# Kernel tuning notes

Measured on AMD Instinct MI355X. Metric: run time of the kernel, lower is better.

The kernel has to match this reference:

```python
import jax, jax.numpy as jnp
import numpy as np

B, T, H = 2, 2048, 1024
DFF = 4 * H        # dense_mlp hidden width
E = 8              # num_experts_temp
TOP_K = 2


def setup_inputs() -> dict:
    key = jax.random.key(0)
    ks = jax.random.split(key, 6)
    s_h = 1.0 / np.sqrt(H)
    s_f = 1.0 / np.sqrt(DFF)
    return {
        "hidden_states": jax.random.normal(ks[0], (B, T, H), dtype=jnp.float32),
        "router_w": jax.random.normal(ks[1], (E, H), dtype=jnp.float32) * s_h,
        "w1": jax.random.normal(ks[2], (E, H, DFF), dtype=jnp.float32) * s_h,
        "b1": jnp.zeros((E, DFF), dtype=jnp.float32),
        "w2": jax.random.normal(ks[3], (E, DFF, H), dtype=jnp.float32) * s_f,
        "b2": jnp.zeros((E, H), dtype=jnp.float32),
    }


def reference(hidden_states, router_w, w1, b1, w2, b2):
    # Router: [B,T,E]
    router_logits = jnp.einsum("bth,eh->bte", hidden_states, router_w)
    topk_vals, topk_idx = jax.lax.top_k(router_logits, TOP_K)        # [B,T,K]
    topk_w = jax.nn.softmax(topk_vals.astype(jnp.float32), axis=-1)
    topk_w = topk_w.astype(hidden_states.dtype)

    # Dense compute of ALL experts (faithful to the original module).
    h = jnp.einsum("bth,ehf->btef", hidden_states, w1) + b1          # [B,T,E,DFF]
    h = jax.nn.gelu(h)
    expert_out = jnp.einsum("btef,efh->bteh", h, w2) + b2            # [B,T,E,H]

    # Gather top-k experts per token and mix.
    topk_out = jnp.take_along_axis(expert_out, topk_idx[..., None], axis=2)  # [B,T,K,H]
    mixed = jnp.sum(topk_out * topk_w[..., None], axis=2)            # [B,T,H]
    return mixed
```

## Files before the change

kernel.cpp:

```cpp
#include <hip/hip_runtime.h>
#include <hip/hip_bf16.h>
#include <stdint.h>

#define AS1 __attribute__((address_space(1)))
#define AS3 __attribute__((address_space(3)))

typedef __bf16 bf16x8 __attribute__((ext_vector_type(8)));
typedef float floatx4 __attribute__((ext_vector_type(4)));

static constexpr int NTOK = 4096;
static constexpr int H    = 1024;
static constexpr int DFF  = 4096;
static constexpr int E    = 8;
static constexpr int BN   = 128;
static constexpr int RB   = 71;

static constexpr size_t OFF_XCS    = 0;
static constexpr size_t OFF_HS     = 18874368;
static constexpr size_t OFF_P      = 94371840;
static constexpr size_t PSZ        = 18874368;
static constexpr size_t OFF_RTIDX  = 169869312;
static constexpr size_t OFF_RTW    = 169902080;
static constexpr size_t OFF_PTOK   = 169934848;
static constexpr size_t OFF_TOKPOS = 169971712;
static constexpr size_t OFF_CNT    = 170004480;
static constexpr size_t WS_NEED    = 170004608;

__device__ __forceinline__ unsigned short f2bf(float f) {
    __bf16 b = (__bf16)f;
    return __builtin_bit_cast(unsigned short, b);
}
__device__ __forceinline__ float bf2f(unsigned short u) {
    unsigned int v = ((unsigned int)u) << 16;
    return __builtin_bit_cast(float, v);
}

__device__ __forceinline__ void gload16(const void* g, void* l) {
    __builtin_amdgcn_global_load_lds((AS1 void*)g, (AS3 void*)l, 16, 0, 0);
}

__device__ __forceinline__ int find_expert_tot(const int* __restrict__ counts, int row, int* tot_out) {
    int e = 0, tot = 0;
#pragma unroll
    for (int i = 0; i < E; ++i) {
        int c = (counts[i] + 127) & ~127;
        if (row >= tot + c) e = i + 1;
        tot += c;
    }
    *tot_out = tot;
    return e;
}
__device__ __forceinline__ int padded_prefix(const int* __restrict__ counts, int e) {
    int o = 0;
#pragma unroll
    for (int i = 0; i < E; ++i) {
        int c = (counts[i] + 127) & ~127;
        o += (i < e) ? c : 0;
    }
    return o;
}

__global__ __launch_bounds__(256) void k_router(const float* __restrict__ x,
                                                const float* __restrict__ rw,
                                                int* __restrict__ rt_idx,
                                                float* __restrict__ rt_w,
                                                int* __restrict__ counts) {
    const int wv = threadIdx.x >> 6, ln = threadIdx.x & 63;
    const int t = blockIdx.x * 4 + wv;
    const float* xr = x + (size_t)t * H + ln * 4;
    float4 xv[4];
#pragma unroll
    for (int c = 0; c < 4; ++c) xv[c] = *(const float4*)(xr + c * 256);
    float lg[E];
#pragma unroll
    for (int e = 0; e < E; ++e) {
        const float* rr = rw + (size_t)e * H + ln * 4;
        float acc = 0.f;
#pragma unroll
        for (int c = 0; c < 4; ++c) {
            float4 rv = *(const float4*)(rr + c * 256);
            acc += xv[c].x * rv.x + xv[c].y * rv.y + xv[c].z * rv.z + xv[c].w * rv.w;
        }
#pragma unroll
        for (int s = 32; s > 0; s >>= 1) acc += __shfl_xor(acc, s, 64);
        lg[e] = acc;
    }
    if (ln == 0) {
        int i0 = 0; float v0 = lg[0];
#pragma unroll
        for (int e = 1; e < E; ++e) if (lg[e] > v0) { v0 = lg[e]; i0 = e; }
        int i1 = -1; float v1 = -INFINITY;
#pragma unroll
        for (int e = 0; e < E; ++e) if (e != i0 && lg[e] > v1) { v1 = lg[e]; i1 = e; }
        float e1 = expf(v1 - v0);
        float inv = 1.f / (1.f + e1);
        rt_idx[2 * t] = i0; rt_idx[2 * t + 1] = i1;
        rt_w[2 * t] = inv;  rt_w[2 * t + 1] = e1 * inv;
        atomicAdd(&counts[i0], 1);
        atomicAdd(&counts[i1], 1);
    }
}

__global__ __launch_bounds__(256) void k_scatter(const int* __restrict__ rt_idx,
                                                 const int* __restrict__ counts,
                                                 int* __restrict__ cursors,
                                                 int* __restrict__ pair_tok,
                                                 int* __restrict__ tok_pos) {
    int t = blockIdx.x * 256 + threadIdx.x;
    if (t >= NTOK) return;
    for (int k = 0; k < 2; ++k) {
        int e = rt_idx[2 * t + k];
        int p = atomicAdd(&cursors[e], 1);
        int pos = padded_prefix(counts, e) + p;
        pair_tok[pos] = t;
        tok_pos[2 * t + k] = pos;
    }
}

__global__ __launch_bounds__(256) void k_gather(const float* __restrict__ x,
                                                const int* __restrict__ counts,
                                                const int* __restrict__ pair_tok,
                                                unsigned short* __restrict__ xcs) {
    int pos = blockIdx.x;
    int tot;
    int e = find_expert_tot(counts, pos, &tot);
    if (pos >= tot) return;
    int off_e = padded_prefix(counts, e);
    bool valid = (pos - off_e) < counts[e];
    int tok = valid ? pair_tok[pos] : 0;
    int k0 = threadIdx.x * 4;
    float4 xv = valid ? *(const float4*)(x + (size_t)tok * H + k0)
                      : make_float4(0.f, 0.f, 0.f, 0.f);
    ushort4 o;
    o.x = f2bf(xv.x); o.y = f2bf(xv.y); o.z = f2bf(xv.z); o.w = f2bf(xv.w);
    int rb = pos >> 7, m = pos & 127;
    size_t idx = (((size_t)(rb * 32 + (k0 >> 5)) * 128 + m) * 32) + (k0 & 31);
    *(ushort4*)(xcs + idx) = o;
}

__global__ __launch_bounds__(256) void k_gemm1(const unsigned short* __restrict__ Xc,
                                               const float* __restrict__ w1,
                                               const int* __restrict__ counts,
                                               const float* __restrict__ b1,
                                               unsigned short* __restrict__ Hs) {
    constexpr int KB = H / 32;
    constexpr int MP = 36;
    constexpr int NB = DFF / BN;
    constexpr int CPX = NB * RB / 8;
    const int bid = blockIdx.x;
    const int t = (bid & 7) * CPX + (bid >> 3);
    const int rb = t / NB;
    const int row = rb * 128;
    int tot;
    const int e = find_expert_tot(counts, row, &tot);
    if (row >= tot) return;
    const int n0 = (t % NB) * BN;

    __shared__ unsigned short smem[4 * 128 * MP];
    unsigned short* lds_a = smem;
    unsigned short* lds_b = smem + 4096;

    const int tid = threadIdx.x;
    const int wv = tid >> 6, ln = tid & 63;
    const int quad = ln >> 4, lr = ln & 15;
    const int wm = (wv & 1) * 64, wn = (wv >> 1) * 64;
    const int bswz = quad ^ ((lr >> 1) & 3);

    const int skq = wv, sn = ln;
    const int sswz = skq ^ ((sn >> 1) & 3);
    const int wb1 = sn * 32 + sswz * 8;
    const int wb2 = wb1 + 2048;

    floatx4 acc[4][4];
#pragma unroll
    for (int i = 0; i < 4; ++i)
#pragma unroll
        for (int j = 0; j < 4; ++j) acc[i][j] = (floatx4){0.f, 0.f, 0.f, 0.f};

    const unsigned short* Atile = Xc + (size_t)rb * KB * 4096;
    const float* Bsrc = w1 + ((size_t)e * H + skq * 8) * DFF + n0 + sn;

    float br[16];
#pragma unroll
    for (int j = 0; j < 8; ++j) {
        br[j]     = Bsrc[(size_t)j * DFF];
        br[8 + j] = Bsrc[(size_t)j * DFF + 64];
    }

    for (int kb = 0; kb < KB; ++kb) {
        __syncthreads();
        {
            union { unsigned short us[8]; uint4 v; } u1, u2;
#pragma unroll
            for (int j = 0; j < 8; ++j) { u1.us[j] = f2bf(br[j]); u2.us[j] = f2bf(br[8 + j]); }
            *(uint4*)(lds_b + wb1) = u1.v;
            *(uint4*)(lds_b + wb2) = u2.v;
        }
        const unsigned short* a_src = Atile + (size_t)kb * 4096 + (wv * 2) * 512 + ln * 8;
        gload16(a_src, &lds_a[(wv * 2) * 512]);
        gload16(a_src + 512, &lds_a[(wv * 2 + 1) * 512]);
        {
            const int kbn = (kb + 1 < KB) ? kb + 1 : kb;
            const float* bs = Bsrc + (size_t)kbn * 32 * DFF;
#pragma unroll
            for (int j = 0; j < 8; ++j) {
                br[j]     = bs[(size_t)j * DFF];
                br[8 + j] = bs[(size_t)j * DFF + 64];
            }
        }
        __syncthreads();
        bf16x8 af[4], bg[4];
#pragma unroll
        for (int i = 0; i < 4; ++i) {
            af[i] = *(const bf16x8*)(lds_a + (wm + i * 16 + lr) * 32 + quad * 8);
            bg[i] = *(const bf16x8*)(lds_b + (wn + i * 16 + lr) * 32 + bswz * 8);
        }
#pragma unroll
        for (int i = 0; i < 4; ++i)
#pragma unroll
            for (int j = 0; j < 4; ++j)
                acc[i][j] = __builtin_amdgcn_mfma_f32_16x16x32_bf16(af[i], bg[j], acc[i][j], 0, 0, 0);
    }

    float bj[4];
#pragma unroll
    for (int j = 0; j < 4; ++j) bj[j] = b1[(size_t)e * DFF + n0 + wn + j * 16 + lr];
    __syncthreads();
#pragma unroll
    for (int j = 0; j < 4; ++j) {
        const int fl = wn + j * 16 + lr;
        const int fb = fl >> 5, f5 = fl & 31;
        unsigned short* dst = smem + fb * (128 * MP) + f5;
#pragma unroll
        for (int i = 0; i < 4; ++i) {
#pragma unroll
            for (int r = 0; r < 4; ++r) {
                const int m = wm + i * 16 + quad * 4 + r;
                float v = acc[i][j][r] + bj[j];
                float u = 0.79788456080286535588f * (v + 0.044715f * v * v * v);
                float ez = __expf(2.f * u);
                float g = v * (1.f - 1.f / (ez + 1.f));
                dst[m * MP] = f2bf(g);
            }
        }
    }
    __syncthreads();
    const size_t hsbase = ((size_t)rb * 128 + (n0 >> 5)) * 4096;
#pragma unroll
    for (int it = 0; it < 8; ++it) {
        const int g = (it * 256 + tid) * 8;
        const int fb = g >> 12, rem = g & 4095, m = rem >> 5, f5 = rem & 31;
        const unsigned short* s = smem + fb * (128 * MP) + m * MP + f5;
        uint2 lo = *(const uint2*)s;
        uint2 hi = *(const uint2*)(s + 4);
        *(uint4*)(Hs + hsbase + (size_t)g) = make_uint4(lo.x, lo.y, hi.x, hi.y);
    }
}

__global__ __launch_bounds__(256) void k_gemm2(const unsigned short* __restrict__ Hs,
                                               const float* __restrict__ w2,
                                               const int* __restrict__ counts,
                                               const float* __restrict__ b2,
                                               unsigned short* __restrict__ Pb) {
    constexpr int KB = DFF / 32;
    constexpr int NSPLIT = 4;
    constexpr int KBS = KB / NSPLIT;
    constexpr int NB = H / BN;
    constexpr int CPX = NB * RB * NSPLIT / 8;
    const int bid = blockIdx.x;
    const int t = (bid & 7) * CPX + (bid >> 3);
    const int nb = t & 7;
    const int rest = t >> 3;
    const int rb = rest % RB;
    const int ks = rest / RB;
    const int row = rb * 128;
    int tot;
    const int e = find_expert_tot(counts, row, &tot);
    if (row >= tot) return;
    const int n0 = nb * BN;

    __shared__ unsigned short smem[8192];
    unsigned short* lds_a = smem;
    unsigned short* lds_b = smem + 4096;

    const int tid = threadIdx.x;
    const int wv = tid >> 6, ln = tid & 63;
    const int quad = ln >> 4, lr = ln & 15;
    const int wm = (wv & 1) * 64, wn = (wv >> 1) * 64;
    const int bswz = quad ^ ((lr >> 1) & 3);

    const int skq = wv, sn = ln;
    const int sswz = skq ^ ((sn >> 1) & 3);
    const int wb1 = sn * 32 + sswz * 8;
    const int wb2 = wb1 + 2048;

    floatx4 acc[4][4];
#pragma unroll
    for (int i = 0; i < 4; ++i)
#pragma unroll
        for (int j = 0; j < 4; ++j) acc[i][j] = (floatx4){0.f, 0.f, 0.f, 0.f};

    const unsigned short* Atile = Hs + ((size_t)rb * KB + ks * KBS) * 4096;
    const float* Bsrc = w2 + ((size_t)e * DFF + ks * KBS * 32 + skq * 8) * H + n0 + sn;

    float br[16];
#pragma unroll
    for (int j = 0; j < 8; ++j) {
        br[j]     = Bsrc[(size_t)j * H];
        br[8 + j] = Bsrc[(size_t)j * H + 64];
    }

    for (int kb = 0; kb < KBS; ++kb) {
        __syncthreads();
        {
            union { unsigned short us[8]; uint4 v; } u1, u2;
#pragma unroll
            for (int j = 0; j < 8; ++j) { u1.us[j] = f2bf(br[j]); u2.us[j] = f2bf(br[8 + j]); }
            *(uint4*)(lds_b + wb1) = u1.v;
            *(uint4*)(lds_b + wb2) = u2.v;
        }
        const unsigned short* a_src = Atile + (size_t)kb * 4096 + (wv * 2) * 512 + ln * 8;
        gload16(a_src, &lds_a[(wv * 2) * 512]);
        gload16(a_src + 512, &lds_a[(wv * 2 + 1) * 512]);
        {
            const int kbn = (kb + 1 < KBS) ? kb + 1 : kb;
            const float* bs = Bsrc + (size_t)kbn * 32 * H;
#pragma unroll
            for (int j = 0; j < 8; ++j) {
                br[j]     = bs[(size_t)j * H];
                br[8 + j] = bs[(size_t)j * H + 64];
            }
        }
        __syncthreads();
        bf16x8 af[4], bg[4];
#pragma unroll
        for (int i = 0; i < 4; ++i) {
            af[i] = *(const bf16x8*)(lds_a + (wm + i * 16 + lr) * 32 + quad * 8);
            bg[i] = *(const bf16x8*)(lds_b + (wn + i * 16 + lr) * 32 + bswz * 8);
        }
#pragma unroll
        for (int i = 0; i < 4; ++i)
#pragma unroll
            for (int j = 0; j < 4; ++j)
                acc[i][j] = __builtin_amdgcn_mfma_f32_16x16x32_bf16(af[i], bg[j], acc[i][j], 0, 0, 0);
    }

    float bj[4];
#pragma unroll
    for (int j = 0; j < 4; ++j)
        bj[j] = (ks == 0) ? b2[(size_t)e * H + n0 + wn + j * 16 + lr] : 0.f;
    unsigned short* P = Pb + (size_t)ks * (PSZ / 2);
#pragma unroll
    for (int i = 0; i < 4; ++i) {
#pragma unroll
        for (int r = 0; r < 4; ++r) {
            const int m = wm + i * 16 + quad * 4 + r;
            unsigned short* rowp = P + (size_t)(rb * 128 + m) * H + n0;
#pragma unroll
            for (int j = 0; j < 4; ++j)
                rowp[wn + j * 16 + lr] = f2bf(acc[i][j][r] + bj[j]);
        }
    }
}

__global__ __launch_bounds__(256) void k_mix(const unsigned short* __restrict__ Pb,
                                             const int* __restrict__ tok_pos,
                                             const float* __restrict__ rt_w,
                                             float* __restrict__ out) {
    const int t = blockIdx.x;
    const int c = threadIdx.x * 4;
    const int p0 = tok_pos[2 * t], p1 = tok_pos[2 * t + 1];
    const float w0 = rt_w[2 * t], w1 = rt_w[2 * t + 1];
    float4 s0 = make_float4(0.f, 0.f, 0.f, 0.f);
    float4 s1 = make_float4(0.f, 0.f, 0.f, 0.f);
#pragma unroll
    for (int q = 0; q < 4; ++q) {
        const unsigned short* P = Pb + (size_t)q * (PSZ / 2);
        ushort4 a = *(const ushort4*)(P + (size_t)p0 * H + c);
        ushort4 b = *(const ushort4*)(P + (size_t)p1 * H + c);
        s0.x += bf2f(a.x); s0.y += bf2f(a.y); s0.z += bf2f(a.z); s0.w += bf2f(a.w);
        s1.x += bf2f(b.x); s1.y += bf2f(b.y); s1.z += bf2f(b.z); s1.w += bf2f(b.w);
    }
    float4 o;
    o.x = w0 * s0.x + w1 * s1.x;
    o.y = w0 * s0.y + w1 * s1.y;
    o.z = w0 * s0.z + w1 * s1.z;
    o.w = w0 * s0.w + w1 * s1.w;
    *(float4*)(out + (size_t)t * H + c) = o;
}

extern "C" void kernel_launch(void* const* d_in, const int* in_sizes, int n_in,
                              void* d_out, int out_size, void* d_ws, size_t ws_size,
                              hipStream_t stream) {
    const float* x  = (const float*)d_in[0];
    const float* rw = (const float*)d_in[1];
    const float* w1 = (const float*)d_in[2];
    const float* b1 = (const float*)d_in[3];
    const float* w2 = (const float*)d_in[4];
    const float* b2 = (const float*)d_in[5];
    float* out = (float*)d_out;
    char* ws = (char*)d_ws;
    if (ws_size < WS_NEED) return;

    unsigned short* XcS = (unsigned short*)(ws + OFF_XCS);
    unsigned short* Hs  = (unsigned short*)(ws + OFF_HS);
    unsigned short* Pb  = (unsigned short*)(ws + OFF_P);
    int*   rt_idx   = (int*)(ws + OFF_RTIDX);
    float* rt_w     = (float*)(ws + OFF_RTW);
    int*   pair_tok = (int*)(ws + OFF_PTOK);
    int*   tok_pos  = (int*)(ws + OFF_TOKPOS);
    int*   cnt      = (int*)(ws + OFF_CNT);
    int*   cur      = cnt + 8;

    hipMemsetAsync(cnt, 0, 128, stream);

    k_router<<<NTOK / 4, 256, 0, stream>>>(x, rw, rt_idx, rt_w, cnt);
    k_scatter<<<NTOK / 256, 256, 0, stream>>>(rt_idx, cnt, cur, pair_tok, tok_pos);
    k_gather<<<RB * 128, 256, 0, stream>>>(x, cnt, pair_tok, XcS);

    k_gemm1<<<(DFF / BN) * RB, 256, 0, stream>>>(XcS, w1, cnt, b1, Hs);
    k_gemm2<<<(H / BN) * RB * 4, 256, 0, stream>>>(Hs, w2, cnt, b2, Pb);

    k_mix<<<NTOK, 256, 0, stream>>>(Pb, tok_pos, rt_w, out);
}
```

Baseline: 665.8 us.

## Double-buffer LDS tiles and register prefetch in both expert GEMM kernels

Replaces the single-buffered K-loop in both expert GEMMs with a ping-pong pipeline. Two LDS buffers hold A and B tiles, and two register sets hold prefetched fp32 weights. The next tile's A gload and B conversion/store overlap the MFMA compute on the current buffer, which halves the number of __syncthreads per K step. This doubles LDS use in gemm2 and raises register pressure, and both kernels now use a hardcoded trip count of 32 K-blocks.

```diff
diff --git a/kernel.cpp b/kernel.cpp
--- a/kernel.cpp
+++ b/kernel.cpp
@@ -138,6 +138,71 @@
     *(ushort4*)(xcs + idx) = o;
 }
 
+#define LOADB(SET, KBN) do {                                                   \
+    const float* bs_ = Bsrc + (size_t)(KBN) * 32 * LDB;                        \
+    _Pragma("unroll")                                                          \
+    for (int j_ = 0; j_ < 8; ++j_) {                                           \
+        brg[SET][j_]     = bs_[(size_t)j_ * LDB];                              \
+        brg[SET][8 + j_] = bs_[(size_t)j_ * LDB + 64];                         \
+    }                                                                          \
+} while (0)
+
+#define STOREB(SET, BUF) do {                                                  \
+    union { unsigned short us[8]; uint4 v; } u1_, u2_;                         \
+    _Pragma("unroll")                                                          \
+    for (int j_ = 0; j_ < 8; ++j_) {                                           \
+        u1_.us[j_] = f2bf(brg[SET][j_]);                                       \
+        u2_.us[j_] = f2bf(brg[SET][8 + j_]);                                   \
+    }                                                                          \
+    *(uint4*)(lds_b + (BUF) * 4096 + wb1) = u1_.v;                             \
+    *(uint4*)(lds_b + (BUF) * 4096 + wb2) = u2_.v;                             \
+} while (0)
+
+#define GLOADA(KB1, BUF) do {                                                  \
+    const unsigned short* a_ = Atile + (size_t)(KB1) * 4096 + (wv * 2) * 512 + ln * 8; \
+    gload16(a_, lds_a + (BUF) * 4096 + (wv * 2) * 512);                        \
+    gload16(a_ + 512, lds_a + (BUF) * 4096 + (wv * 2 + 1) * 512);              \
+} while (0)
+
+#define COMPUTE(BUF) do {                                                      \
+    bf16x8 af_[4], bg_[4];                                                     \
+    _Pragma("unroll")                                                          \
+    for (int i_ = 0; i_ < 4; ++i_) {                                           \
+        af_[i_] = *(const bf16x8*)(lds_a + (BUF) * 4096 + (wm + i_ * 16 + lr) * 32 + quad * 8); \
+        bg_[i_] = *(const bf16x8*)(lds_b + (BUF) * 4096 + (wn + i_ * 16 + lr) * 32 + bswz * 8); \
+    }                                                                          \
+    _Pragma("unroll")                                                          \
+    for (int i_ = 0; i_ < 4; ++i_)                                             \
+        _Pragma("unroll")                                                      \
+        for (int j_ = 0; j_ < 4; ++j_)                                         \
+            acc[i_][j_] = __builtin_amdgcn_mfma_f32_16x16x32_bf16(af_[i_], bg_[j_], acc[i_][j_], 0, 0, 0); \
+} while (0)
+
+#define GEMM_PIPELINE()                                                        \
+    LOADB(0, 0);                                                               \
+    STOREB(0, 0);                       \
+    GLOADA(0, 0);                                                              \
+    LOADB(1, 1);                                                               \
+    __syncthreads();                   \
+    for (int t2_ = 0; t2_ < 15; ++t2_) {                                       \
+        const int t_ = t2_ * 2;                                                \
+        GLOADA(t_ + 1, 1);            \
+        STOREB(1, 1);                            \
+        LOADB(0, t_ + 2);                               \
+        COMPUTE(0);                                               \
+        __syncthreads();                                                       \
+        GLOADA(t_ + 2, 0);                                                     \
+        STOREB(0, 0);                                                          \
+        LOADB(1, t_ + 3);                          \
+        COMPUTE(1);                                           \
+        __syncthreads();                                                       \
+    }                                                                          \
+    GLOADA(31, 1);                                                             \
+    STOREB(1, 1);                                          \
+    COMPUTE(0);                                                   \
+    __syncthreads();                                                           \
+    COMPUTE(1);
+
 __global__ __launch_bounds__(256) void k_gemm1(const unsigned short* __restrict__ Xc,
                                                const float* __restrict__ w1,
                                                const int* __restrict__ counts,
@@ -147,6 +212,7 @@
     constexpr int MP = 36;
     constexpr int NB = DFF / BN;
     constexpr int CPX = NB * RB / 8;
+    constexpr int LDB = DFF;
     const int bid = blockIdx.x;
     const int t = (bid & 7) * CPX + (bid >> 3);
     const int rb = t / NB;
@@ -158,7 +224,7 @@
 
     __shared__ unsigned short smem[4 * 128 * MP];
     unsigned short* lds_a = smem;
-    unsigned short* lds_b = smem + 4096;
+    unsigned short* lds_b = smem + 8192;
 
     const int tid = threadIdx.x;
     const int wv = tid >> 6, ln = tid & 63;
@@ -179,48 +245,9 @@
 
     const unsigned short* Atile = Xc + (size_t)rb * KB * 4096;
     const float* Bsrc = w1 + ((size_t)e * H + skq * 8) * DFF + n0 + sn;
-
-    float br[16];
-#pragma unroll
-    for (int j = 0; j < 8; ++j) {
-        br[j]     = Bsrc[(size_t)j * DFF];
-        br[8 + j] = Bsrc[(size_t)j * DFF + 64];
-    }
-
-    for (int kb = 0; kb < KB; ++kb) {
-        __syncthreads();
-        {
-            union { unsigned short us[8]; uint4 v; } u1, u2;
-#pragma unroll
-            for (int j = 0; j < 8; ++j) { u1.us[j] = f2bf(br[j]); u2.us[j] = f2bf(br[8 + j]); }
-            *(uint4*)(lds_b + wb1) = u1.v;
-            *(uint4*)(lds_b + wb2) = u2.v;
-        }
-        const unsigned short* a_src = Atile + (size_t)kb * 4096 + (wv * 2) * 512 + ln * 8;
-        gload16(a_src, &lds_a[(wv * 2) * 512]);
-        gload16(a_src + 512, &lds_a[(wv * 2 + 1) * 512]);
-        {
-            const int kbn = (kb + 1 < KB) ? kb + 1 : kb;
-            const float* bs = Bsrc + (size_t)kbn * 32 * DFF;
-#pragma unroll
-            for (int j = 0; j < 8; ++j) {
-                br[j]     = bs[(size_t)j * DFF];
-                br[8 + j] = bs[(size_t)j * DFF + 64];
-            }
-        }
-        __syncthreads();
-        bf16x8 af[4], bg[4];
-#pragma unroll
-        for (int i = 0; i < 4; ++i) {
-            af[i] = *(const bf16x8*)(lds_a + (wm + i * 16 + lr) * 32 + quad * 8);
-            bg[i] = *(const bf16x8*)(lds_b + (wn + i * 16 + lr) * 32 + bswz * 8);
-        }
-#pragma unroll
-        for (int i = 0; i < 4; ++i)
-#pragma unroll
-            for (int j = 0; j < 4; ++j)
-                acc[i][j] = __builtin_amdgcn_mfma_f32_16x16x32_bf16(af[i], bg[j], acc[i][j], 0, 0, 0);
-    }
+    float brg[2][16];
+
+    GEMM_PIPELINE();
 
     float bj[4];
 #pragma unroll
@@ -262,11 +289,12 @@
                                                const int* __restrict__ counts,
                                                const float* __restrict__ b2,
                                                unsigned short* __restrict__ Pb) {
-    constexpr int KB = DFF / 32;
+    constexpr int KBT = DFF / 32;
     constexpr int NSPLIT = 4;
-    constexpr int KBS = KB / NSPLIT;
+    constexpr int KBS = KBT / NSPLIT;
     constexpr int NB = H / BN;
     constexpr int CPX = NB * RB * NSPLIT / 8;
+    constexpr int LDB = H;
     const int bid = blockIdx.x;
     const int t = (bid & 7) * CPX + (bid >> 3);
     const int nb = t & 7;
@@ -279,9 +307,9 @@
     if (row >= tot) return;
     const int n0 = nb * BN;
 
-    __shared__ unsigned short smem[8192];
+    __shared__ unsigned short smem[16384];
     unsigned short* lds_a = smem;
-    unsigned short* lds_b = smem + 4096;
+    unsigned short* lds_b = smem + 8192;
 
     const int tid = threadIdx.x;
     const int wv = tid >> 6, ln = tid & 63;
@@ -300,50 +328,11 @@
 #pragma unroll
         for (int j = 0; j < 4; ++j) acc[i][j] = (floatx4){0.f, 0.f, 0.f, 0.f};
 
-    const unsigned short* Atile = Hs + ((size_t)rb * KB + ks * KBS) * 4096;
+    const unsigned short* Atile = Hs + ((size_t)rb * KBT + ks * KBS) * 4096;
     const float* Bsrc = w2 + ((size_t)e * DFF + ks * KBS * 32 + skq * 8) * H + n0 + sn;
-
-    float br[16];
-#pragma unroll
-    for (int j = 0; j < 8; ++j) {
-        br[j]     = Bsrc[(size_t)j * H];
-        br[8 + j] = Bsrc[(size_t)j * H + 64];
-    }
-
-    for (int kb = 0; kb < KBS; ++kb) {
-        __syncthreads();
-        {
-            union { unsigned short us[8]; uint4 v; } u1, u2;
-#pragma unroll
-            for (int j = 0; j < 8; ++j) { u1.us[j] = f2bf(br[j]); u2.us[j] = f2bf(br[8 + j]); }
-            *(uint4*)(lds_b + wb1) = u1.v;
-            *(uint4*)(lds_b + wb2) = u2.v;
-        }
-        const unsigned short* a_src = Atile + (size_t)kb * 4096 + (wv * 2) * 512 + ln * 8;
-        gload16(a_src, &lds_a[(wv * 2) * 512]);
-        gload16(a_src + 512, &lds_a[(wv * 2 + 1) * 512]);
-        {
-            const int kbn = (kb + 1 < KBS) ? kb + 1 : kb;
-            const float* bs = Bsrc + (size_t)kbn * 32 * H;
-#pragma unroll
-            for (int j = 0; j < 8; ++j) {
-                br[j]     = bs[(size_t)j * H];
-                br[8 + j] = bs[(size_t)j * H + 64];
-            }
-        }
-        __syncthreads();
-        bf16x8 af[4], bg[4];
-#pragma unroll
-        for (int i = 0; i < 4; ++i) {
-            af[i] = *(const bf16x8*)(lds_a + (wm + i * 16 + lr) * 32 + quad * 8);
-            bg[i] = *(const bf16x8*)(lds_b + (wn + i * 16 + lr) * 32 + bswz * 8);
-        }
-#pragma unroll
-        for (int i = 0; i < 4; ++i)
-#pragma unroll
-            for (int j = 0; j < 4; ++j)
-                acc[i][j] = __builtin_amdgcn_mfma_f32_16x16x32_bf16(af[i], bg[j], acc[i][j], 0, 0, 0);
-    }
+    float brg[2][16];
+
+    GEMM_PIPELINE();
 
     float bj[4];
 #pragma unroll
```

Result: slower. 749.3 us (+12.5%).

## Halve gemm2 split-K and drop XCD-aware block remapping

Applied to the files above, without the earlier changes.

Cuts the split-K factor of the second expert GEMM from 4 to 2, so each block covers twice the K range. The grid shrinks accordingly and k_mix now sums two partials instead of four. It also removes the XCD-interleaved block index swizzle in both GEMMs and uses blockIdx.x directly. The aim is less partial-output traffic and reduction work, at the cost of fewer blocks, less parallelism and possibly worse L2 locality across XCDs.

```diff
diff --git a/kernel.cpp b/kernel.cpp
--- a/kernel.cpp
+++ b/kernel.cpp
@@ -146,9 +146,8 @@
     constexpr int KB = H / 32;
     constexpr int MP = 36;
     constexpr int NB = DFF / BN;
-    constexpr int CPX = NB * RB / 8;
-    const int bid = blockIdx.x;
-    const int t = (bid & 7) * CPX + (bid >> 3);
+    constexpr int LDB = DFF;
+    const int t = blockIdx.x;
     const int rb = t / NB;
     const int row = rb * 128;
     int tot;
@@ -178,13 +177,13 @@
         for (int j = 0; j < 4; ++j) acc[i][j] = (floatx4){0.f, 0.f, 0.f, 0.f};
 
     const unsigned short* Atile = Xc + (size_t)rb * KB * 4096;
-    const float* Bsrc = w1 + ((size_t)e * H + skq * 8) * DFF + n0 + sn;
+    const float* Bsrc = w1 + ((size_t)e * H + skq * 8) * LDB + n0 + sn;
 
     float br[16];
 #pragma unroll
     for (int j = 0; j < 8; ++j) {
-        br[j]     = Bsrc[(size_t)j * DFF];
-        br[8 + j] = Bsrc[(size_t)j * DFF + 64];
+        br[j]     = Bsrc[(size_t)j * LDB];
+        br[8 + j] = Bsrc[(size_t)j * LDB + 64];
     }
 
     for (int kb = 0; kb < KB; ++kb) {
@@ -201,11 +200,11 @@
         gload16(a_src + 512, &lds_a[(wv * 2 + 1) * 512]);
         {
             const int kbn = (kb + 1 < KB) ? kb + 1 : kb;
-            const float* bs = Bsrc + (size_t)kbn * 32 * DFF;
+            const float* bs = Bsrc + (size_t)kbn * 32 * LDB;
 #pragma unroll
             for (int j = 0; j < 8; ++j) {
-                br[j]     = bs[(size_t)j * DFF];
-                br[8 + j] = bs[(size_t)j * DFF + 64];
+                br[j]     = bs[(size_t)j * LDB];
+                br[8 + j] = bs[(size_t)j * LDB + 64];
             }
         }
         __syncthreads();
@@ -262,13 +261,12 @@
                                                const int* __restrict__ counts,
                                                const float* __restrict__ b2,
                                                unsigned short* __restrict__ Pb) {
-    constexpr int KB = DFF / 32;
-    constexpr int NSPLIT = 4;
-    constexpr int KBS = KB / NSPLIT;
+    constexpr int KBT = DFF / 32;
+    constexpr int NSPLIT = 2;
+    constexpr int KBS = KBT / NSPLIT;
     constexpr int NB = H / BN;
-    constexpr int CPX = NB * RB * NSPLIT / 8;
-    const int bid = blockIdx.x;
-    const int t = (bid & 7) * CPX + (bid >> 3);
+    constexpr int LDB = H;
+    const int t = blockIdx.x;
     const int nb = t & 7;
     const int rest = t >> 3;
     const int rb = rest % RB;
@@ -300,14 +298,14 @@
 #pragma unroll
         for (int j = 0; j < 4; ++j) acc[i][j] = (floatx4){0.f, 0.f, 0.f, 0.f};
 
-    const unsigned short* Atile = Hs + ((size_t)rb * KB + ks * KBS) * 4096;
-    const float* Bsrc = w2 + ((size_t)e * DFF + ks * KBS * 32 + skq * 8) * H + n0 + sn;
+    const unsigned short* Atile = Hs + ((size_t)rb * KBT + ks * KBS) * 4096;
+    const float* Bsrc = w2 + ((size_t)e * DFF + ks * KBS * 32 + skq * 8) * LDB + n0 + sn;
 
     float br[16];
 #pragma unroll
     for (int j = 0; j < 8; ++j) {
-        br[j]     = Bsrc[(size_t)j * H];
-        br[8 + j] = Bsrc[(size_t)j * H + 64];
+        br[j]     = Bsrc[(size_t)j * LDB];
+        br[8 + j] = Bsrc[(size_t)j * LDB + 64];
     }
 
     for (int kb = 0; kb < KBS; ++kb) {
@@ -324,11 +322,11 @@
         gload16(a_src + 512, &lds_a[(wv * 2 + 1) * 512]);
         {
             const int kbn = (kb + 1 < KBS) ? kb + 1 : kb;
-            const float* bs = Bsrc + (size_t)kbn * 32 * H;
+            const float* bs = Bsrc + (size_t)kbn * 32 * LDB;
 #pragma unroll
             for (int j = 0; j < 8; ++j) {
-                br[j]     = bs[(size_t)j * H];
-                br[8 + j] = bs[(size_t)j * H + 64];
+                br[j]     = bs[(size_t)j * LDB];
+                br[8 + j] = bs[(size_t)j * LDB + 64];
             }
         }
         __syncthreads();
@@ -374,7 +372,7 @@
     float4 s0 = make_float4(0.f, 0.f, 0.f, 0.f);
     float4 s1 = make_float4(0.f, 0.f, 0.f, 0.f);
 #pragma unroll
-    for (int q = 0; q < 4; ++q) {
+    for (int q = 0; q < 2; ++q) {
         const unsigned short* P = Pb + (size_t)q * (PSZ / 2);
         ushort4 a = *(const ushort4*)(P + (size_t)p0 * H + c);
         ushort4 b = *(const ushort4*)(P + (size_t)p1 * H + c);
@@ -419,7 +417,7 @@
     k_gather<<<RB * 128, 256, 0, stream>>>(x, cnt, pair_tok, XcS);
 
     k_gemm1<<<(DFF / BN) * RB, 256, 0, stream>>>(XcS, w1, cnt, b1, Hs);
-    k_gemm2<<<(H / BN) * RB * 4, 256, 0, stream>>>(Hs, w2, cnt, b2, Pb);
+    k_gemm2<<<(H / BN) * RB * 2, 256, 0, stream>>>(Hs, w2, cnt, b2, Pb);
 
     k_mix<<<NTOK, 256, 0, stream>>>(Pb, tok_pos, rt_w, out);
 }
```

New measurement: 687.0 us. 3.2% more time.
